# Kernel optimization log

Measured on AMD Instinct MI355X. Metric: run time of the kernel, lower is better.

The kernel has to match this reference:

```python
import jax, jax.numpy as jnp
import numpy as np

K = 5        # kernel_size per pseudo-dim
DIM = 2      # pseudo-coordinate dimensionality
K2 = K * K   # total kernel weight matrices
N_NODES = 50000


def spline_basis(edge_attr):
    """Open B-spline basis, degree=1, dim=2. Returns basis [E,4], weight_index [E,4]."""
    v = edge_attr * (K - 1)                      # [E,2], pseudo in [0,1]
    lo = jnp.floor(v)
    frac = v - lo                                # [E,2]
    lo = lo.astype(jnp.int32)
    fac = jnp.stack([1.0 - frac, frac], axis=-1)                 # [E,2,2] (dim, bit)
    idx = jnp.clip(lo[..., None] + jnp.arange(2), 0, K - 1)      # [E,2,2]
    b0 = jnp.array([0, 1, 0, 1])  # bit for dim 0, per spline term
    b1 = jnp.array([0, 0, 1, 1])  # bit for dim 1
    basis = fac[:, 0, b0] * fac[:, 1, b1]        # [E,4]
    wi = idx[:, 0, b0] * K + idx[:, 1, b1]       # [E,4] flat kernel index
    return basis, wi


def spline_conv(x, src, dst, basis, wi, W, root, bias, n_nodes):
    """SplineConv with mean aggregation, root weight and bias.
    x:[N,Fin] W:[K2,Fin,Fout] root:[Fin,Fout] bias:[Fout]"""
    E = src.shape[0]
    K2_, Fin, Fout = W.shape
    # scatter the 4 sparse basis values into a dense per-edge kernel-coeff matrix [E,K2]
    coeff = jnp.zeros((E, K2_), x.dtype).at[jnp.arange(E)[:, None], wi].add(basis)
    xj = x[src]                                  # gather source features [E,Fin]
    msg = jnp.zeros((E, Fout), x.dtype)
    for k in range(K2_):                         # fixed small loop over 25 kernels
        msg = msg + coeff[:, k:k + 1] * (xj @ W[k])
    agg = jax.ops.segment_sum(msg, dst, num_segments=n_nodes)    # [N,Fout]
    deg = jax.ops.segment_sum(jnp.ones((E,), x.dtype), dst, num_segments=n_nodes)
    agg = agg / jnp.clip(deg, 1.0)[:, None]      # mean aggregation
    return agg + x @ root + bias


def setup_inputs() -> dict:
    key = jax.random.key(0)
    ks = jax.random.split(key, 9)
    E = 800000
    Fin, H, C = 64, 16, 7
    x = jax.random.normal(ks[0], (N_NODES, Fin), dtype=jnp.float32)
    edge_index = jax.random.randint(ks[1], (2, E), 0, N_NODES, dtype=jnp.int64)
    edge_attr = jax.random.uniform(ks[2], (E, DIM), dtype=jnp.float32)
    s1 = 1.0 / np.sqrt(Fin)
    s2 = 1.0 / np.sqrt(H)
    W1 = jax.random.uniform(ks[3], (K2, Fin, H), jnp.float32, -s1, s1)
    root1 = jax.random.uniform(ks[4], (Fin, H), jnp.float32, -s1, s1)
    bias1 = jax.random.uniform(ks[5], (H,), jnp.float32, -s1, s1)
    W2 = jax.random.uniform(ks[6], (K2, H, C), jnp.float32, -s2, s2)
    root2 = jax.random.uniform(ks[7], (H, C), jnp.float32, -s2, s2)
    bias2 = jax.random.uniform(ks[8], (C,), jnp.float32, -s2, s2)
    return {"x": x, "edge_index": edge_index, "edge_attr": edge_attr,
            "W1": W1, "root1": root1, "bias1": bias1,
            "W2": W2, "root2": root2, "bias2": bias2}


def reference(x, edge_index, edge_attr, W1, root1, bias1, W2, root2, bias2):
    src = edge_index[0]
    dst = edge_index[1]
    basis, wi = spline_basis(edge_attr)
    h = jax.nn.relu(spline_conv(x, src, dst, basis, wi, W1, root1, bias1, N_NODES))
    # dropout(p=0.6) is identity in eval mode
    out = spline_conv(h, src, dst, basis, wi, W2, root2, bias2, N_NODES)
    return jax.nn.log_softmax(out, axis=1)
```

## Files before the change

kernel.cpp:

```cpp
#include <hip/hip_runtime.h>

#define KK2 25
#define FIN 64
#define HH 16
#define CC 7

#define SCAN_VPT 4
#define SCAN_BLK 256
#define SCAN_CHUNK (SCAN_VPT * SCAN_BLK)

__device__ inline unsigned short f2bf(float f) {
    unsigned u = __float_as_uint(f);
    return (unsigned short)((u + 0x7FFFu + ((u >> 16) & 1u)) >> 16);
}
__device__ inline float bf2f(unsigned short b) {
    return __uint_as_float(((unsigned)b) << 16);
}

__global__ void k_hist(const int* __restrict__ ei, int* __restrict__ cnt, int E) {
    int e = blockIdx.x * 256 + threadIdx.x;
    if (e < E) atomicAdd(&cnt[ei[E + e]], 1);
}

__global__ void k_bsum(const int* __restrict__ cnt, int* __restrict__ bsum, int N) {
    int b = blockIdx.x, t = threadIdx.x;
    int base = b * SCAN_CHUNK + t * SCAN_VPT;
    int s = 0;
#pragma unroll
    for (int j = 0; j < SCAN_VPT; j++) {
        int i = base + j;
        if (i < N) s += cnt[i];
    }
#pragma unroll
    for (int d = 1; d < 64; d <<= 1) s += __shfl_xor(s, d, 64);
    __shared__ int sd[SCAN_BLK / 64];
    if ((t & 63) == 0) sd[t >> 6] = s;
    __syncthreads();
    if (t == 0) {
        int tot = 0;
        for (int w = 0; w < SCAN_BLK / 64; w++) tot += sd[w];
        bsum[b] = tot;
    }
}

__global__ void k_bscan(const int* __restrict__ bsum, int* __restrict__ boff, int nblk) {
    int t = threadIdx.x;
    __shared__ int sd[256];
    int v = (t < nblk) ? bsum[t] : 0;
    sd[t] = v;
    __syncthreads();
    for (int off = 1; off < 256; off <<= 1) {
        int u = (t >= off) ? sd[t - off] : 0;
        __syncthreads();
        sd[t] += u;
        __syncthreads();
    }
    boff[t] = sd[t] - v;
}

__global__ void k_sfin(const int* __restrict__ cnt, const int* __restrict__ boff,
                       int* __restrict__ rowStart, int* __restrict__ cursor, int N) {
    int b = blockIdx.x, t = threadIdx.x;
    int base = b * SCAN_CHUNK + t * SCAN_VPT;
    int v[SCAN_VPT];
    int s = 0;
#pragma unroll
    for (int j = 0; j < SCAN_VPT; j++) {
        int i = base + j;
        v[j] = (i < N) ? cnt[i] : 0;
        s += v[j];
    }
    __shared__ int sd[SCAN_BLK];
    sd[t] = s;
    __syncthreads();
    for (int off = 1; off < SCAN_BLK; off <<= 1) {
        int u = (t >= off) ? sd[t - off] : 0;
        __syncthreads();
        sd[t] += u;
        __syncthreads();
    }
    int run = sd[t] - s + boff[b];
#pragma unroll
    for (int j = 0; j < SCAN_VPT; j++) {
        int i = base + j;
        if (i < N) {
            rowStart[i] = run;
            cursor[i] = run;
            run += v[j];
            if (i == N - 1) rowStart[N] = run;
        }
    }
}

__global__ void k_scatter(const float* __restrict__ attr, const int* __restrict__ ei,
                          int* __restrict__ cursor, uint4* __restrict__ rec, int E) {
    int e = blockIdx.x * 256 + threadIdx.x;
    if (e >= E) return;
    float v0 = attr[2 * e] * 4.0f, v1 = attr[2 * e + 1] * 4.0f;
    float l0 = floorf(v0), l1 = floorf(v1);
    float f0 = v0 - l0, f1 = v1 - l1;
    int i0 = (int)l0, i1 = (int)l1;
    int i0a = min(max(i0, 0), 4), i0b = min(max(i0 + 1, 0), 4);
    int i1a = min(max(i1, 0), 4);
    float bx = (1.0f - f0) * (1.0f - f1);
    float by = f0 * (1.0f - f1);
    float bz = (1.0f - f0) * f1;
    float bw = f0 * f1;
    unsigned pA = (unsigned)(i0a * 5 + i1a);
    unsigned pB = (unsigned)(i0b * 5 + i1a);
    int s = ei[e], d = ei[E + e];
    int pos = atomicAdd(&cursor[d], 1);
    uint4 r;
    r.x = (unsigned)f2bf(bx) | ((unsigned)f2bf(by) << 16);
    r.y = (unsigned)f2bf(bz) | ((unsigned)f2bf(bw) << 16);
    r.z = (unsigned)s;
    r.w = pA | (pB << 8);
    rec[pos] = r;
}

__global__ void k_prepW(const float* __restrict__ W1, const float* __restrict__ W2,
                        float* __restrict__ B1t, float* __restrict__ W2p) {
    int tid = blockIdx.x * 256 + threadIdx.x;
    if (tid < KK2 * FIN * HH) {
        int c = tid >> 6, i = tid & 63;
        int k = c >> 4, h = c & 15;
        B1t[tid] = W1[(k * FIN + i) * HH + h];
    }
    if (tid < KK2 * HH * 8) {
        int k = tid >> 7, r = tid & 127;
        int i = r >> 3, c = r & 7;
        W2p[tid] = (c < CC) ? W2[(k * HH + i) * CC + c] : 0.0f;
    }
}

__global__ void k_y1(const float* __restrict__ x, const float* __restrict__ B1t,
                     unsigned short* __restrict__ y1n, int N, int nbl) {
    __shared__ uint4 sh[4][2][144];
    int i0 = blockIdx.x / nbl;
    int nwin = blockIdx.x % nbl;
    int n = nwin * 256 + threadIdx.x;
    int wv = threadIdx.x >> 6, lane = threadIdx.x & 63;
    bool active = (n < N);
    float4 xr[16];
    if (active) {
        const float4* xp = (const float4*)(x + (size_t)n * 64);
#pragma unroll
        for (int i = 0; i < 16; i++) xr[i] = xp[i];
    }
    int nwb = nwin * 256 + wv * 64;
    int validf = min(64, max(0, N - nwb)) * 4;

    for (int i1 = 0; i1 < 5; i1++) {
        int k = i0 * 5 + i1;
        const float* B = B1t + k * 16 * 64;
        unsigned tmp[8];
        if (active) {
#pragma unroll
            for (int h4 = 0; h4 < 4; h4++) {
                float a0 = 0, a1 = 0, a2 = 0, a3 = 0;
                const float4* b0 = (const float4*)(B + (h4 * 4 + 0) * 64);
                const float4* b1 = (const float4*)(B + (h4 * 4 + 1) * 64);
                const float4* b2 = (const float4*)(B + (h4 * 4 + 2) * 64);
                const float4* b3 = (const float4*)(B + (h4 * 4 + 3) * 64);
#pragma unroll
                for (int i = 0; i < 16; i++) {
                    float4 xi = xr[i];
                    float4 v0 = b0[i], v1 = b1[i], v2 = b2[i], v3 = b3[i];
                    a0 += xi.x * v0.x + xi.y * v0.y + xi.z * v0.z + xi.w * v0.w;
                    a1 += xi.x * v1.x + xi.y * v1.y + xi.z * v1.z + xi.w * v1.w;
                    a2 += xi.x * v2.x + xi.y * v2.y + xi.z * v2.z + xi.w * v2.w;
                    a3 += xi.x * v3.x + xi.y * v3.y + xi.z * v3.z + xi.w * v3.w;
                }
                tmp[h4 * 2 + 0] = (unsigned)f2bf(a0) | ((unsigned)f2bf(a1) << 16);
                tmp[h4 * 2 + 1] = (unsigned)f2bf(a2) | ((unsigned)f2bf(a3) << 16);
            }
        } else {
#pragma unroll
            for (int j = 0; j < 8; j++) tmp[j] = 0;
        }
        int slot = i1 & 1;
        int i0e = lane * 2, i1e = lane * 2 + 1;
        sh[wv][slot][i0e + (i0e >> 3)] = make_uint4(tmp[0], tmp[1], tmp[2], tmp[3]);
        sh[wv][slot][i1e + (i1e >> 3)] = make_uint4(tmp[4], tmp[5], tmp[6], tmp[7]);
        __syncthreads();
        if (i1 >= 1) {
            int p = i0 * 5 + (i1 - 1);
            uint4* g4 = (uint4*)y1n;
#pragma unroll
            for (int j = 0; j < 4; j++) {
                int f = j * 64 + lane;
                if (f < validf) {
                    int m = f >> 2, q = f & 3;
                    int idx = m * 2 + (q & 1);
                    int ss = (q < 2) ? (slot ^ 1) : slot;
                    g4[(size_t)(nwb + m) * 100 + p * 4 + q] = sh[wv][ss][idx + (idx >> 3)];
                }
            }
        }
        if (i1 == 4) {
            int p = i0 * 5 + 4;
            uint4* g4 = (uint4*)y1n;
#pragma unroll
            for (int j = 0; j < 4; j++) {
                int f = j * 64 + lane;
                if (f < validf) {
                    int m = f >> 2, q = f & 3;
                    int idx = m * 2 + (q & 1);
                    g4[(size_t)(nwb + m) * 100 + p * 4 + q] = sh[wv][slot][idx + (idx >> 3)];
                }
            }
        }
        __syncthreads();
    }
}

__global__ void k_agg1u(const int* __restrict__ rowStart, const uint4* __restrict__ rec,
                        const unsigned short* __restrict__ y1n, const float* __restrict__ x,
                        const float* __restrict__ root1, const float* __restrict__ bias1,
                        float* __restrict__ h1, int N) {
    int n = blockIdx.x * 4 + (threadIdx.x >> 6);
    if (n >= N) return;
    int lane = threadIdx.x & 63;
    int sub = lane >> 4, h = lane & 15;
    int start = rowStart[n], end = rowStart[n + 1];
    float acc0 = 0.0f, acc1 = 0.0f;
    int i = start + sub;
    for (; i + 4 < end; i += 8) {
        uint4 r0 = rec[i];
        uint4 r1 = rec[i + 4];
        {
            int s = (int)r0.z;
            unsigned w = r0.w;
            const unsigned short* rA = y1n + (size_t)s * 800 + (w & 255u) * 32;
            const unsigned short* rB = y1n + (size_t)s * 800 + ((w >> 8) & 255u) * 32;
            acc0 += bf2f((unsigned short)(r0.x & 0xffffu)) * bf2f(rA[h])
                  + bf2f((unsigned short)(r0.y & 0xffffu)) * bf2f(rA[16 + h])
                  + bf2f((unsigned short)(r0.x >> 16)) * bf2f(rB[h])
                  + bf2f((unsigned short)(r0.y >> 16)) * bf2f(rB[16 + h]);
        }
        {
            int s = (int)r1.z;
            unsigned w = r1.w;
            const unsigned short* rA = y1n + (size_t)s * 800 + (w & 255u) * 32;
            const unsigned short* rB = y1n + (size_t)s * 800 + ((w >> 8) & 255u) * 32;
            acc1 += bf2f((unsigned short)(r1.x & 0xffffu)) * bf2f(rA[h])
                  + bf2f((unsigned short)(r1.y & 0xffffu)) * bf2f(rA[16 + h])
                  + bf2f((unsigned short)(r1.x >> 16)) * bf2f(rB[h])
                  + bf2f((unsigned short)(r1.y >> 16)) * bf2f(rB[16 + h]);
        }
    }
    for (; i < end; i += 4) {
        uint4 r = rec[i];
        int s = (int)r.z;
        unsigned w = r.w;
        const unsigned short* rA = y1n + (size_t)s * 800 + (w & 255u) * 32;
        const unsigned short* rB = y1n + (size_t)s * 800 + ((w >> 8) & 255u) * 32;
        acc0 += bf2f((unsigned short)(r.x & 0xffffu)) * bf2f(rA[h])
              + bf2f((unsigned short)(r.y & 0xffffu)) * bf2f(rA[16 + h])
              + bf2f((unsigned short)(r.x >> 16)) * bf2f(rB[h])
              + bf2f((unsigned short)(r.y >> 16)) * bf2f(rB[16 + h]);
    }
    float acc = acc0 + acc1;
    acc += __shfl_xor(acc, 16, 64);
    acc += __shfl_xor(acc, 32, 64);
    float inv = 1.0f / (float)max(end - start, 1);
    float rv = acc * inv + bias1[h];
    const float* xrow = x + (size_t)n * 64;
#pragma unroll 8
    for (int ii = 0; ii < 64; ii++) rv += xrow[ii] * root1[ii * 16 + h];
    rv = fmaxf(rv, 0.0f);
    if (lane < 16) h1[(size_t)n * 16 + h] = rv;
}

__global__ void k_y2(const float* __restrict__ h1, const float* __restrict__ W2p,
                     unsigned short* __restrict__ y2Tb, int N, int nbl) {
    int kg = blockIdx.x / nbl;
    int n = (blockIdx.x % nbl) * 256 + threadIdx.x;
    if (n >= N) return;
    float hreg[16];
    const float4* hp = (const float4*)(h1 + (size_t)n * 16);
#pragma unroll
    for (int j = 0; j < 4; j++) {
        float4 v = hp[j];
        hreg[4 * j] = v.x; hreg[4 * j + 1] = v.y;
        hreg[4 * j + 2] = v.z; hreg[4 * j + 3] = v.w;
    }
#pragma unroll
    for (int dk = 0; dk < 5; dk++) {
        int k = kg * 5 + dk;
        float z[8] = {0, 0, 0, 0, 0, 0, 0, 0};
        const float4* wp = (const float4*)(W2p + k * 128);
#pragma unroll
        for (int i = 0; i < 16; i++) {
            float hi = hreg[i];
            float4 lo = wp[2 * i], hv = wp[2 * i + 1];
            z[0] += hi * lo.x; z[1] += hi * lo.y; z[2] += hi * lo.z; z[3] += hi * lo.w;
            z[4] += hi * hv.x; z[5] += hi * hv.y; z[6] += hi * hv.z; z[7] += hi * hv.w;
        }
        uint4 p;
        p.x = (unsigned)f2bf(z[0]) | ((unsigned)f2bf(z[1]) << 16);
        p.y = (unsigned)f2bf(z[2]) | ((unsigned)f2bf(z[3]) << 16);
        p.z = (unsigned)f2bf(z[4]) | ((unsigned)f2bf(z[5]) << 16);
        p.w = (unsigned)f2bf(z[6]) | ((unsigned)f2bf(z[7]) << 16);
        *(uint4*)(y2Tb + ((size_t)k * N + n) * 8) = p;
    }
}

__global__ void k_agg2f(const int* __restrict__ rowStart, const uint4* __restrict__ rec,
                        const unsigned short* __restrict__ y2Tb, const float* __restrict__ h1,
                        const float* __restrict__ root2, const float* __restrict__ bias2,
                        float* __restrict__ out, int N) {
    int n = blockIdx.x * 4 + (threadIdx.x >> 6);
    if (n >= N) return;
    int lane = threadIdx.x & 63;
    int sub = lane >> 3, c = lane & 7;
    int start = rowStart[n], end = rowStart[n + 1];
    float acc = 0.0f;
    size_t NN = (size_t)N;
    for (int i = start + sub; i < end; i += 8) {
        uint4 r = rec[i];
        float bx = bf2f((unsigned short)(r.x & 0xffffu));
        float by = bf2f((unsigned short)(r.x >> 16));
        float bz = bf2f((unsigned short)(r.y & 0xffffu));
        float bw = bf2f((unsigned short)(r.y >> 16));
        int s = (int)r.z;
        unsigned pA = r.w & 255u, pB = (r.w >> 8) & 255u;
        unsigned i1a = pA % 5u;
        unsigned d = (i1a < 4u) ? 1u : 0u;
        acc += bx * bf2f(y2Tb[(pA * NN + s) * 8 + c]);
        acc += by * bf2f(y2Tb[(pB * NN + s) * 8 + c]);
        acc += bz * bf2f(y2Tb[((pA + d) * NN + s) * 8 + c]);
        acc += bw * bf2f(y2Tb[((pB + d) * NN + s) * 8 + c]);
    }
    acc += __shfl_xor(acc, 8, 64);
    acc += __shfl_xor(acc, 16, 64);
    acc += __shfl_xor(acc, 32, 64);
    float inv = 1.0f / (float)max(end - start, 1);
    float z;
    if (c < CC) {
        z = acc * inv + bias2[c];
        const float* hrow = h1 + (size_t)n * 16;
#pragma unroll
        for (int i = 0; i < 16; i++) z += hrow[i] * root2[i * CC + c];
    } else {
        z = -1e30f;
    }
    float m = z;
    m = fmaxf(m, __shfl_xor(m, 1, 64));
    m = fmaxf(m, __shfl_xor(m, 2, 64));
    m = fmaxf(m, __shfl_xor(m, 4, 64));
    float ex = (c < CC) ? expf(z - m) : 0.0f;
    float ssum = ex;
    ssum += __shfl_xor(ssum, 1, 64);
    ssum += __shfl_xor(ssum, 2, 64);
    ssum += __shfl_xor(ssum, 4, 64);
    float ls = logf(ssum);
    if (lane < CC) out[(size_t)n * 7 + c] = z - m - ls;
}

extern "C" void kernel_launch(void* const* d_in, const int* in_sizes, int n_in,
                              void* d_out, int out_size, void* d_ws, size_t ws_size,
                              hipStream_t stream) {
    const float* x     = (const float*)d_in[0];
    const int*   ei    = (const int*)d_in[1];
    const float* attr  = (const float*)d_in[2];
    const float* W1    = (const float*)d_in[3];
    const float* root1 = (const float*)d_in[4];
    const float* bias1 = (const float*)d_in[5];
    const float* W2    = (const float*)d_in[6];
    const float* root2 = (const float*)d_in[7];
    const float* bias2 = (const float*)d_in[8];
    float* out = (float*)d_out;

    int N = in_sizes[0] / FIN;
    int E = in_sizes[1] / 2;

    char* w = (char*)d_ws;
    size_t off = 0;
    auto alloc = [&](size_t bytes) -> void* {
        void* p = w + off;
        off += (bytes + 255) & ~(size_t)255;
        return p;
    };
    int*      cnt      = (int*)alloc((size_t)N * 4);
    int*      rowStart = (int*)alloc((size_t)(N + 1) * 4);
    int*      cursor   = (int*)alloc((size_t)N * 4);
    int*      bsum     = (int*)alloc(260 * 4);
    int*      boff     = (int*)alloc(260 * 4);
    uint4*    rec      = (uint4*)alloc((size_t)E * 16);
    float*    h1       = (float*)alloc((size_t)N * 64);
    float*    B1t      = (float*)alloc((size_t)KK2 * FIN * HH * 4);
    float*    W2p      = (float*)alloc((size_t)KK2 * HH * 8 * 4);
    unsigned short* y1n  = (unsigned short*)alloc((size_t)N * 800 * 2);
    unsigned short* y2Tb = y1n;
    (void)ws_size; (void)n_in; (void)out_size;

    hipMemsetAsync(cnt, 0, (size_t)N * 4, stream);

    int ebl = (E + 255) / 256;
    int nbl = (N + 255) / 256;
    int sblk = (N + SCAN_CHUNK - 1) / SCAN_CHUNK;

    k_hist<<<ebl, 256, 0, stream>>>(ei, cnt, E);
    k_bsum<<<sblk, SCAN_BLK, 0, stream>>>(cnt, bsum, N);
    k_bscan<<<1, 256, 0, stream>>>(bsum, boff, sblk);
    k_sfin<<<sblk, SCAN_BLK, 0, stream>>>(cnt, boff, rowStart, cursor, N);
    k_scatter<<<ebl, 256, 0, stream>>>(attr, ei, cursor, rec, E);
    k_prepW<<<(KK2 * FIN * HH + 255) / 256, 256, 0, stream>>>(W1, W2, B1t, W2p);
    k_y1<<<5 * nbl, 256, 0, stream>>>(x, B1t, y1n, N, nbl);
    k_agg1u<<<(N + 3) / 4, 256, 0, stream>>>(rowStart, rec, y1n, x, root1, bias1, h1, N);
    k_y2<<<5 * nbl, 256, 0, stream>>>(h1, W2p, y2Tb, N, nbl);
    k_agg2f<<<(N + 3) / 4, 256, 0, stream>>>(rowStart, rec, y2Tb, h1, root2, bias2, out, N);
}
```

Before: 287.0 us.

## Fuse layer-2 node transform into layer-1 aggregation with node-major layout

Removes the separate k_y2 kernel and computes each node's 25x8 layer-2 transform inside k_agg1u, broadcasting the 16 hidden values through wave shuffles. The y2 buffer moves from kernel-major [k][N][8] to node-major [N][256], so the four gathers per edge in k_agg2f land in one 512-byte row of the source node. This saves a kernel launch and a reread of h1, and should improve locality in the second gather. In exchange, k_agg1u does extra per-node work and reads the W2p weights per lane, and it keeps a separate y2 allocation instead of reusing the y1 buffer.

```diff
diff --git a/kernel.cpp b/kernel.cpp
--- a/kernel.cpp
+++ b/kernel.cpp
@@ -217,7 +217,8 @@
 __global__ void k_agg1u(const int* __restrict__ rowStart, const uint4* __restrict__ rec,
                         const unsigned short* __restrict__ y1n, const float* __restrict__ x,
                         const float* __restrict__ root1, const float* __restrict__ bias1,
-                        float* __restrict__ h1, int N) {
+                        const float* __restrict__ W2p, float* __restrict__ h1,
+                        unsigned short* __restrict__ y2n, int N) {
     int n = blockIdx.x * 4 + (threadIdx.x >> 6);
     if (n >= N) return;
     int lane = threadIdx.x & 63;
@@ -270,44 +271,27 @@
     for (int ii = 0; ii < 64; ii++) rv += xrow[ii] * root1[ii * 16 + h];
     rv = fmaxf(rv, 0.0f);
     if (lane < 16) h1[(size_t)n * 16 + h] = rv;
-}
-
-__global__ void k_y2(const float* __restrict__ h1, const float* __restrict__ W2p,
-                     unsigned short* __restrict__ y2Tb, int N, int nbl) {
-    int kg = blockIdx.x / nbl;
-    int n = (blockIdx.x % nbl) * 256 + threadIdx.x;
-    if (n >= N) return;
-    float hreg[16];
-    const float4* hp = (const float4*)(h1 + (size_t)n * 16);
-#pragma unroll
-    for (int j = 0; j < 4; j++) {
-        float4 v = hp[j];
-        hreg[4 * j] = v.x; hreg[4 * j + 1] = v.y;
-        hreg[4 * j + 2] = v.z; hreg[4 * j + 3] = v.w;
-    }
-#pragma unroll
-    for (int dk = 0; dk < 5; dk++) {
-        int k = kg * 5 + dk;
-        float z[8] = {0, 0, 0, 0, 0, 0, 0, 0};
-        const float4* wp = (const float4*)(W2p + k * 128);
-#pragma unroll
-        for (int i = 0; i < 16; i++) {
-            float hi = hreg[i];
-            float4 lo = wp[2 * i], hv = wp[2 * i + 1];
-            z[0] += hi * lo.x; z[1] += hi * lo.y; z[2] += hi * lo.z; z[3] += hi * lo.w;
-            z[4] += hi * hv.x; z[5] += hi * hv.y; z[6] += hi * hv.z; z[7] += hi * hv.w;
-        }
-        uint4 p;
-        p.x = (unsigned)f2bf(z[0]) | ((unsigned)f2bf(z[1]) << 16);
-        p.y = (unsigned)f2bf(z[2]) | ((unsigned)f2bf(z[3]) << 16);
-        p.z = (unsigned)f2bf(z[4]) | ((unsigned)f2bf(z[5]) << 16);
-        p.w = (unsigned)f2bf(z[6]) | ((unsigned)f2bf(z[7]) << 16);
-        *(uint4*)(y2Tb + ((size_t)k * N + n) * 8) = p;
+
+    float hbc[16];
+#pragma unroll
+    for (int ii = 0; ii < 16; ii++) hbc[ii] = __shfl(rv, ii, 64);
+    unsigned short* yrow = y2n + (size_t)n * 256;
+    int kq = lane >> 3, c = lane & 7;
+#pragma unroll
+    for (int kk = 0; kk < 4; kk++) {
+        int k = kk * 8 + kq;
+        float z = 0.0f;
+        if (k < KK2) {
+            const float* wp = W2p + k * 128 + c;
+#pragma unroll
+            for (int ii = 0; ii < 16; ii++) z += hbc[ii] * wp[ii * 8];
+        }
+        yrow[kk * 64 + lane] = f2bf(z);
     }
 }
 
 __global__ void k_agg2f(const int* __restrict__ rowStart, const uint4* __restrict__ rec,
-                        const unsigned short* __restrict__ y2Tb, const float* __restrict__ h1,
+                        const unsigned short* __restrict__ y2n, const float* __restrict__ h1,
                         const float* __restrict__ root2, const float* __restrict__ bias2,
                         float* __restrict__ out, int N) {
     int n = blockIdx.x * 4 + (threadIdx.x >> 6);
@@ -316,7 +300,6 @@
     int sub = lane >> 3, c = lane & 7;
     int start = rowStart[n], end = rowStart[n + 1];
     float acc = 0.0f;
-    size_t NN = (size_t)N;
     for (int i = start + sub; i < end; i += 8) {
         uint4 r = rec[i];
         float bx = bf2f((unsigned short)(r.x & 0xffffu));
@@ -325,12 +308,12 @@
         float bw = bf2f((unsigned short)(r.y >> 16));
         int s = (int)r.z;
         unsigned pA = r.w & 255u, pB = (r.w >> 8) & 255u;
-        unsigned i1a = pA % 5u;
-        unsigned d = (i1a < 4u) ? 1u : 0u;
-        acc += bx * bf2f(y2Tb[(pA * NN + s) * 8 + c]);
-        acc += by * bf2f(y2Tb[(pB * NN + s) * 8 + c]);
-        acc += bz * bf2f(y2Tb[((pA + d) * NN + s) * 8 + c]);
-        acc += bw * bf2f(y2Tb[((pB + d) * NN + s) * 8 + c]);
+        unsigned d = ((pA % 5u) < 4u) ? 1u : 0u;
+        const unsigned short* yrow = y2n + (size_t)s * 256;
+        acc += bx * bf2f(yrow[pA * 8 + c]);
+        acc += by * bf2f(yrow[pB * 8 + c]);
+        acc += bz * bf2f(yrow[(pA + d) * 8 + c]);
+        acc += bw * bf2f(yrow[(pB + d) * 8 + c]);
     }
     acc += __shfl_xor(acc, 8, 64);
     acc += __shfl_xor(acc, 16, 64);
@@ -391,8 +374,8 @@
     float*    h1       = (float*)alloc((size_t)N * 64);
     float*    B1t      = (float*)alloc((size_t)KK2 * FIN * HH * 4);
     float*    W2p      = (float*)alloc((size_t)KK2 * HH * 8 * 4);
-    unsigned short* y1n  = (unsigned short*)alloc((size_t)N * 800 * 2);
-    unsigned short* y2Tb = y1n;
+    unsigned short* y2n = (unsigned short*)alloc((size_t)N * 256 * 2);
+    unsigned short* y1n = (unsigned short*)alloc((size_t)N * 800 * 2);
     (void)ws_size; (void)n_in; (void)out_size;
 
     hipMemsetAsync(cnt, 0, (size_t)N * 4, stream);
@@ -408,7 +391,7 @@
     k_scatter<<<ebl, 256, 0, stream>>>(attr, ei, cursor, rec, E);
     k_prepW<<<(KK2 * FIN * HH + 255) / 256, 256, 0, stream>>>(W1, W2, B1t, W2p);
     k_y1<<<5 * nbl, 256, 0, stream>>>(x, B1t, y1n, N, nbl);
-    k_agg1u<<<(N + 3) / 4, 256, 0, stream>>>(rowStart, rec, y1n, x, root1, bias1, h1, N);
-    k_y2<<<5 * nbl, 256, 0, stream>>>(h1, W2p, y2Tb, N, nbl);
-    k_agg2f<<<(N + 3) / 4, 256, 0, stream>>>(rowStart, rec, y2Tb, h1, root2, bias2, out, N);
-}
+    k_agg1u<<<(N + 3) / 4, 256, 0, stream>>>(rowStart, rec, y1n, x, root1, bias1,
+                                             W2p, h1, y2n, N);
+    k_agg2f<<<(N + 3) / 4, 256, 0, stream>>>(rowStart, rec, y2n, h1, root2, bias2, out, N);
+}
```

After: 298.3 us. 1.04x slower.
